# Kernel tuning notes

Hardware: AMD Instinct MI355X
Metric: run time of the kernel (lower is better)

Reference implementation:

```python
import jax, jax.numpy as jnp
import numpy as np

GROUP_SIZE = 32


def setup_inputs() -> dict:
    key = jax.random.key(0)
    act = jax.random.normal(key, (4, 4096, 4096), dtype=jnp.float32)
    return {"act": act}


def reference(act):
    G = GROUP_SIZE
    D = act.shape[-1]
    n_groups = D // G  # D divisible by G per input_specs
    lead = act.shape[:-1]
    ag = act.reshape(*lead, n_groups, G)  # [..., n_groups, G]

    # Global per-group amax over ALL leading dims and the within-group dim
    # (matches torch: a_slice.abs().max() with no dim argument).
    reduce_axes = tuple(range(ag.ndim - 2)) + (ag.ndim - 1,)
    max_abs = jnp.max(jnp.abs(ag), axis=reduce_axes)  # [n_groups]

    # e = floor(log2(max_abs)), with e=0 when max_abs == 0.
    safe = jnp.where(max_abs > 0, max_abs, 1.0)
    exps = jnp.where(max_abs > 0, jnp.floor(jnp.log2(safe)), 0.0)
    exps = jax.lax.stop_gradient(exps)  # exponents are constants (.item() in torch)

    scale = jnp.exp2(exps)  # [n_groups], 2**e
    s = scale[..., :, None]  # broadcast over group elements
    ratio = jnp.clip(jnp.abs(ag) / s, 0.0, 1.0)
    mantissa = jnp.round(ratio * 8.0) / 8.0  # 3-bit mantissa grid
    q = jnp.sign(ag) * s * mantissa
    return q.reshape(act.shape), exps
```

## Files before the change

### kernel.cpp

```cpp
#include <hip/hip_runtime.h>
#include <cmath>

#define NELEM      (4ull * 4096ull * 4096ull)
#define NV4        (NELEM / 4ull)
#define NGROUPS    128
#define P1_BLOCKS  512
#define P1_THREADS 1024

typedef float v4f __attribute__((ext_vector_type(4)));

__global__ void __launch_bounds__(P1_THREADS)
pass1_max(const float4* __restrict__ in, unsigned int* __restrict__ partials) {
    __shared__ unsigned int smax[NGROUPS];
    const int tid = threadIdx.x;
    if (tid < NGROUPS) smax[tid] = 0u;
    __syncthreads();

    const size_t idx    = (size_t)blockIdx.x * P1_THREADS + tid;
    const size_t stride = (size_t)P1_BLOCKS * P1_THREADS;
    const int g = tid >> 3;

    float m = 0.0f;
    #pragma unroll 4
    for (size_t i = idx; i < NV4; i += stride) {
        float4 v = in[i];
        m = fmaxf(m, fmaxf(fmaxf(fabsf(v.x), fabsf(v.y)),
                           fmaxf(fabsf(v.z), fabsf(v.w))));
    }
    atomicMax(&smax[g], __float_as_uint(m));
    __syncthreads();
    if (tid < NGROUPS)
        partials[(size_t)blockIdx.x * NGROUPS + tid] = smax[tid];
}

__global__ void __launch_bounds__(1024)
reduce_scales(const unsigned int* __restrict__ partials,
              float* __restrict__ exps_out, float2* __restrict__ scales) {
    __shared__ unsigned int red[NGROUPS];
    const int tid = threadIdx.x;
    if (tid < NGROUPS) red[tid] = 0u;
    __syncthreads();

    const int g = tid & 127;
    const int c = tid >> 7;
    unsigned int m = 0u;
    #pragma unroll 8
    for (int b = c * 64; b < c * 64 + 64; ++b)
        m = max(m, partials[(size_t)b * NGROUPS + g]);
    atomicMax(&red[g], m);
    __syncthreads();

    if (tid < NGROUPS) {
        const float mf = __uint_as_float(red[tid]);
        int e = 0;
        if (mf > 0.0f) {
            int e2;
            (void)frexpf(mf, &e2);
            e = e2 - 1;
        }
        exps_out[tid] = (float)e;
        scales[tid] = make_float2(ldexpf(1.0f, e - 3),
                                  ldexpf(1.0f, -e));
    }
}

__global__ void __launch_bounds__(256)
pass2_quant(const float4* __restrict__ in, float4* __restrict__ out,
            const float2* __restrict__ scales) {
    __shared__ float2 ssc[NGROUPS];
    const int tid = threadIdx.x;
    if (tid < NGROUPS) ssc[tid] = scales[tid];
    __syncthreads();

    const size_t idx    = (size_t)blockIdx.x * blockDim.x + tid;
    const size_t stride = (size_t)gridDim.x * blockDim.x;
    const int g = (int)((idx & 1023u) >> 3);
    const float qstep = ssc[g].x;
    const float inv_s = ssc[g].y;

    for (size_t i = idx; i < NV4; i += stride) {
        float4 v = in[i];
        v4f q;
        q.x = copysignf(rintf(fminf(fabsf(v.x) * inv_s, 1.0f) * 8.0f) * qstep, v.x);
        q.y = copysignf(rintf(fminf(fabsf(v.y) * inv_s, 1.0f) * 8.0f) * qstep, v.y);
        q.z = copysignf(rintf(fminf(fabsf(v.z) * inv_s, 1.0f) * 8.0f) * qstep, v.z);
        q.w = copysignf(rintf(fminf(fabsf(v.w) * inv_s, 1.0f) * 8.0f) * qstep, v.w);
        __builtin_nontemporal_store(q, (v4f*)&out[i]);
    }
}

extern "C" void kernel_launch(void* const* d_in, const int* in_sizes, int n_in,
                              void* d_out, int out_size, void* d_ws, size_t ws_size,
                              hipStream_t stream) {
    const float* act = (const float*)d_in[0];
    float* q_out    = (float*)d_out;
    float* exps_out = q_out + NELEM;

    unsigned int* partials = (unsigned int*)d_ws;
    float2* scales = (float2*)((char*)d_ws + P1_BLOCKS * NGROUPS * sizeof(unsigned int));

    pass1_max<<<P1_BLOCKS, P1_THREADS, 0, stream>>>((const float4*)act, partials);
    reduce_scales<<<1, 1024, 0, stream>>>(partials, exps_out, scales);
    pass2_quant<<<2048, 256, 0, stream>>>((const float4*)act, (float4*)q_out, scales);
}
```

Before: 132.9 us.

## Fuse max, scale reduction and quantization into one cooperative kernel

Replaces the three launches (partial max, scale reduction, quantize) with one cooperative kernel that uses a grid-wide sync between the max phase and the quantize phase. Each block owns a fixed residue of the 128 groups (block index mod 4) and reduces only the partials for its 32 groups, so every block computes its own scales and no separate reduction launch is needed. The second pass rereads the same slice of the input that the block just read, which may raise cache hits on the 256MB input. The cost is a grid barrier and the requirement that all 1024 blocks be co-resident.

New measurement: 238.3 us. 1.79x slower.

```diff
diff --git a/kernel.cpp b/kernel.cpp
--- a/kernel.cpp
+++ b/kernel.cpp
@@ -1,84 +1,76 @@
 #include <hip/hip_runtime.h>
+#include <hip/hip_cooperative_groups.h>
 #include <cmath>
 
-#define NELEM      (4ull * 4096ull * 4096ull)
-#define NV4        (NELEM / 4ull)
-#define NGROUPS    128
-#define P1_BLOCKS  512
-#define P1_THREADS 1024
+namespace cg = cooperative_groups;
+
+#define NELEM    (4ull * 4096ull * 4096ull)
+#define NV4      (NELEM / 4ull)
+#define NGROUPS  128
+#define GRID     1024
+#define BLK      256
+#define NTHREADS ((size_t)GRID * BLK)
+#define ITERS    (NV4 / NTHREADS)
 
 typedef float v4f __attribute__((ext_vector_type(4)));
 
-__global__ void __launch_bounds__(P1_THREADS)
-pass1_max(const float4* __restrict__ in, unsigned int* __restrict__ partials) {
-    __shared__ unsigned int smax[NGROUPS];
+__global__ void __launch_bounds__(BLK, 4)
+fused_quant(const float4* __restrict__ in, float4* __restrict__ out,
+            float* __restrict__ exps_out, unsigned int* __restrict__ partials) {
+    __shared__ unsigned int smax[32];
+    __shared__ float2 ssc[32];
+
     const int tid = threadIdx.x;
-    if (tid < NGROUPS) smax[tid] = 0u;
+    const int bid = blockIdx.x;
+    const int res = bid & 3;
+    const int l   = tid >> 3;
+
+    if (tid < 32) smax[tid] = 0u;
     __syncthreads();
 
-    const size_t idx    = (size_t)blockIdx.x * P1_THREADS + tid;
-    const size_t stride = (size_t)P1_BLOCKS * P1_THREADS;
-    const int g = tid >> 3;
+    const size_t idx = (size_t)bid * BLK + tid;
 
     float m = 0.0f;
     #pragma unroll 4
-    for (size_t i = idx; i < NV4; i += stride) {
-        float4 v = in[i];
+    for (int t = 0; t < (int)ITERS; ++t) {
+        float4 v = in[idx + (size_t)t * NTHREADS];
         m = fmaxf(m, fmaxf(fmaxf(fabsf(v.x), fabsf(v.y)),
                            fmaxf(fabsf(v.z), fabsf(v.w))));
     }
-    atomicMax(&smax[g], __float_as_uint(m));
+    atomicMax(&smax[l], __float_as_uint(m));
     __syncthreads();
-    if (tid < NGROUPS)
-        partials[(size_t)blockIdx.x * NGROUPS + tid] = smax[tid];
-}
+    if (tid < 32) partials[bid * 32 + tid] = smax[tid];
 
-__global__ void __launch_bounds__(1024)
-reduce_scales(const unsigned int* __restrict__ partials,
-              float* __restrict__ exps_out, float2* __restrict__ scales) {
-    __shared__ unsigned int red[NGROUPS];
-    const int tid = threadIdx.x;
-    if (tid < NGROUPS) red[tid] = 0u;
+    cg::this_grid().sync();
+
+    if (tid < 32) smax[tid] = 0u;
+    __syncthreads();
+    {
+        const int c = tid & 7;
+        unsigned int mm = 0u;
+        #pragma unroll
+        for (int k = 0; k < 32; ++k) {
+            const int b2 = res + 4 * (c * 32 + k);
+            mm = max(mm, partials[b2 * 32 + l]);
+        }
+        atomicMax(&smax[l], mm);
+    }
+    __syncthreads();
+    if (tid < 32) {
+        const float mf = __uint_as_float(smax[tid]);
+        int e = 0;
+        if (mf > 0.0f) { int e2; (void)frexpf(mf, &e2); e = e2 - 1; }
+        ssc[tid] = make_float2(ldexpf(1.0f, e - 3),
+                               ldexpf(1.0f, -e));
+        if (bid < 4) exps_out[res * 32 + tid] = (float)e;
+    }
     __syncthreads();
 
-    const int g = tid & 127;
-    const int c = tid >> 7;
-    unsigned int m = 0u;
-    #pragma unroll 8
-    for (int b = c * 64; b < c * 64 + 64; ++b)
-        m = max(m, partials[(size_t)b * NGROUPS + g]);
-    atomicMax(&red[g], m);
-    __syncthreads();
+    const float qstep = ssc[l].x;
+    const float inv_s = ssc[l].y;
 
-    if (tid < NGROUPS) {
-        const float mf = __uint_as_float(red[tid]);
-        int e = 0;
-        if (mf > 0.0f) {
-            int e2;
-            (void)frexpf(mf, &e2);
-            e = e2 - 1;
-        }
-        exps_out[tid] = (float)e;
-        scales[tid] = make_float2(ldexpf(1.0f, e - 3),
-                                  ldexpf(1.0f, -e));
-    }
-}
-
-__global__ void __launch_bounds__(256)
-pass2_quant(const float4* __restrict__ in, float4* __restrict__ out,
-            const float2* __restrict__ scales) {
-    __shared__ float2 ssc[NGROUPS];
-    const int tid = threadIdx.x;
-    if (tid < NGROUPS) ssc[tid] = scales[tid];
-    __syncthreads();
-
-    const size_t idx    = (size_t)blockIdx.x * blockDim.x + tid;
-    const size_t stride = (size_t)gridDim.x * blockDim.x;
-    const int g = (int)((idx & 1023u) >> 3);
-    const float qstep = ssc[g].x;
-    const float inv_s = ssc[g].y;
-
-    for (size_t i = idx; i < NV4; i += stride) {
+    for (int t = 0; t < (int)ITERS; ++t) {
+        const size_t i = idx + (size_t)t * NTHREADS;
         float4 v = in[i];
         v4f q;
         q.x = copysignf(rintf(fminf(fabsf(v.x) * inv_s, 1.0f) * 8.0f) * qstep, v.x);
@@ -92,14 +84,12 @@
 extern "C" void kernel_launch(void* const* d_in, const int* in_sizes, int n_in,
                               void* d_out, int out_size, void* d_ws, size_t ws_size,
                               hipStream_t stream) {
-    const float* act = (const float*)d_in[0];
-    float* q_out    = (float*)d_out;
-    float* exps_out = q_out + NELEM;
+    const float4* act = (const float4*)d_in[0];
+    float4* q_out     = (float4*)d_out;
+    float* exps_out   = (float*)d_out + NELEM;
+    unsigned int* partials = (unsigned int*)d_ws;
 
-    unsigned int* partials = (unsigned int*)d_ws;
-    float2* scales = (float2*)((char*)d_ws + P1_BLOCKS * NGROUPS * sizeof(unsigned int));
-
-    pass1_max<<<P1_BLOCKS, P1_THREADS, 0, stream>>>((const float4*)act, partials);
-    reduce_scales<<<1, 1024, 0, stream>>>(partials, exps_out, scales);
-    pass2_quant<<<2048, 256, 0, stream>>>((const float4*)act, (float4*)q_out, scales);
+    void* args[] = { (void*)&act, (void*)&q_out, (void*)&exps_out, (void*)&partials };
+    hipLaunchCooperativeKernel(reinterpret_cast<void*>(fused_quant),
+                               dim3(GRID), dim3(BLK), args, 0, stream);
 }
```
